# Optimization experiments

Hardware: AMD Instinct MI355X
Metric: run time of the kernel (lower is better)

## Reference

```python
import jax, jax.numpy as jnp
import numpy as np
from jax import lax

K_NEIGHBORS = 8  # num_neighbors
EPS_BN = 1e-5

def _bn(x, g, b, axes):
    # training-mode batch norm over `axes`, channel axis = 1
    m = jnp.mean(x, axis=axes, keepdims=True)
    v = jnp.var(x, axis=axes, keepdims=True)
    shp = [1] * x.ndim; shp[1] = x.shape[1]
    return (x - m) / jnp.sqrt(v + EPS_BN) * g.reshape(shp) + b.reshape(shp)

def _conv(x, w, b):
    y = lax.conv_general_dilated(x, w, (1, 1), 'SAME',
                                 dimension_numbers=('NCHW', 'OIHW', 'NCHW'))
    return y + b[None, :, None, None]

def setup_inputs() -> dict:
    key = jax.random.key(0)
    ks = jax.random.split(key, 20)
    B, C, H, W = 64, 200, 27, 27
    D, F, NC, HID = 64, 9, 16, 128
    inp = {
        'x': jax.random.normal(ks[0], (B, C, H, W), jnp.float32),
        'conv1_w': jax.random.normal(ks[1], (32, C, 3, 3), jnp.float32) * 0.02,
        'conv1_b': jnp.zeros((32,), jnp.float32),
        'bn1_g': jnp.ones((32,), jnp.float32), 'bn1_b': jnp.zeros((32,), jnp.float32),
        'conv2_w': jax.random.normal(ks[2], (64, 32, 3, 3), jnp.float32) * 0.05,
        'conv2_b': jnp.zeros((64,), jnp.float32),
        'bn2_g': jnp.ones((64,), jnp.float32), 'bn2_b': jnp.zeros((64,), jnp.float32),
        'conv3_w': jax.random.normal(ks[3], (D, 64, 3, 3), jnp.float32) * 0.05,
        'conv3_b': jnp.zeros((D,), jnp.float32),
        'bn3_g': jnp.ones((D,), jnp.float32), 'bn3_b': jnp.zeros((D,), jnp.float32),
        'w_self': jax.random.normal(ks[4], (D, D), jnp.float32) * (2.0 / (2 * D)) ** 0.5,
        'w_nb': jax.random.normal(ks[5], (D, D), jnp.float32) * (2.0 / (2 * D)) ** 0.5,
        'gkan_bias': jnp.zeros((D,), jnp.float32),
        'kan_a': jax.random.normal(ks[6], (D, 3), jnp.float32) * 0.1,
        'kan_b': jax.random.normal(ks[7], (D, 2), jnp.float32) * 0.1,
        'gkan_bn_g': jnp.ones((D,), jnp.float32), 'gkan_bn_b': jnp.zeros((D,), jnp.float32),
        'centers': jax.random.normal(ks[8], (D, F), jnp.float32),
        'gamma': jnp.ones((D, F), jnp.float32) * 0.5,
        'attn_w1': jax.random.normal(ks[9], (D // 4, D), jnp.float32) * 0.1,
        'attn_b1': jnp.zeros((D // 4,), jnp.float32),
        'attn_w2': jax.random.normal(ks[10], (D, D // 4), jnp.float32) * 0.1,
        'attn_b2': jnp.zeros((D,), jnp.float32),
        'fa_bn_g': jnp.ones((D,), jnp.float32), 'fa_bn_b': jnp.zeros((D,), jnp.float32),
        'fc1_w': jax.random.normal(ks[11], (HID, D), jnp.float32) * 0.1,
        'fc1_b': jnp.zeros((HID,), jnp.float32),
        'cls_bn_g': jnp.ones((HID,), jnp.float32), 'cls_bn_b': jnp.zeros((HID,), jnp.float32),
        'fc2_w': jax.random.normal(ks[12], (NC, HID), jnp.float32) * 0.1,
        'fc2_b': jnp.zeros((NC,), jnp.float32),
    }
    return inp

def _forward(x, conv1_w, conv1_b, bn1_g, bn1_b, conv2_w, conv2_b, bn2_g, bn2_b,
             conv3_w, conv3_b, bn3_g, bn3_b, w_self, w_nb, gkan_bias, kan_a, kan_b,
             gkan_bn_g, gkan_bn_b, centers, gamma, attn_w1, attn_b1, attn_w2, attn_b2,
             fa_bn_g, fa_bn_b, fc1_w, fc1_b, cls_bn_g, cls_bn_b, fc2_w, fc2_b):
    # --- CNN encoder ---
    h = jax.nn.relu(_bn(_conv(x, conv1_w, conv1_b), bn1_g, bn1_b, (0, 2, 3)))
    h = jax.nn.relu(_bn(_conv(h, conv2_w, conv2_b), bn2_g, bn2_b, (0, 2, 3)))
    h = jax.nn.relu(_bn(_conv(h, conv3_w, conv3_b), bn3_g, bn3_b, (0, 2, 3)))
    # --- tokenize: [B,D,H,W] -> [B,N,D] ---
    B, D, H, W = h.shape
    N = H * W
    t = h.reshape(B, D, N).transpose(0, 2, 1)
    # --- kNN graph (vectorized topk + scatter) ---
    xx = jnp.sum(t * t, axis=-1, keepdims=True)               # [B,N,1]
    xy = jnp.einsum('bnd,bmd->bnm', t, t)                     # [B,N,N]
    dist = jnp.maximum(xx - 2.0 * xy + xx.transpose(0, 2, 1), 0.0)
    k = min(K_NEIGHBORS + 1, N)
    _, idx = lax.top_k(-dist, k)                              # smallest-k, [B,N,k]
    adj = jnp.zeros((B, N, N), t.dtype).at[
        jnp.arange(B)[:, None, None], jnp.arange(N)[None, :, None], idx[:, :, 1:]
    ].set(1.0)
    deg = jnp.sum(adj, axis=-1) + 1e-6                        # [B,N]
    dinv = deg ** -0.5
    adj_norm = dinv[:, :, None] * adj * dinv[:, None, :] + jnp.eye(N, dtype=t.dtype)[None]
    # --- GKAN graph conv ---
    h_self = t @ w_self                                       # [B,N,D]
    h_nb = jnp.einsum('bnm,bmd->bnd', adj_norm, t @ w_nb)
    g = h_self + h_nb + gkan_bias
    g2 = g * g
    num = kan_a[:, 0] + kan_a[:, 1] * g + kan_a[:, 2] * g2
    den = 1.0 + jnp.abs(kan_b[:, 0] * g + kan_b[:, 1] * g2)
    g = num / (den + 1e-8)
    g = _bn(g.transpose(0, 2, 1), gkan_bn_g, gkan_bn_b, (0, 2)).transpose(0, 2, 1)
    # --- Fuzzy attention (RBF membership; logsumexp(log(v+1e-10)) == sum(v+1e-10)) ---
    d2 = (g[..., None] - centers[None, None]) ** 2            # [B,N,D,F]
    rbf = jnp.sum(jnp.exp(-jnp.abs(gamma)[None, None] * d2) + 1e-10, axis=-1)
    a1 = jax.nn.relu(rbf @ attn_w1.T + attn_b1)
    attn = jax.nn.sigmoid(a1 @ attn_w2.T + attn_b2)
    g = g * attn + g
    g = _bn(g.transpose(0, 2, 1), fa_bn_g, fa_bn_b, (0, 2)).transpose(0, 2, 1)
    # dropout: identity in eval
    # --- global pool + classifier ---
    p = 0.5 * jnp.mean(g, axis=1) + 0.5 * jnp.max(g, axis=1)  # [B,D]
    c = p @ fc1_w.T + fc1_b
    c = jax.nn.relu(_bn(c, cls_bn_g, cls_bn_b, (0,)))
    return c @ fc2_w.T + fc2_b

def reference(x, conv1_w, conv1_b, bn1_g, bn1_b, conv2_w, conv2_b, bn2_g, bn2_b,
              conv3_w, conv3_b, bn3_g, bn3_b, w_self, w_nb, gkan_bias, kan_a, kan_b,
              gkan_bn_g, gkan_bn_b, centers, gamma, attn_w1, attn_b1, attn_w2, attn_b2,
              fa_bn_g, fa_bn_b, fc1_w, fc1_b, cls_bn_g, cls_bn_b, fc2_w, fc2_b):
    return _forward(x, conv1_w, conv1_b, bn1_g, bn1_b, conv2_w, conv2_b, bn2_g, bn2_b,
                    conv3_w, conv3_b, bn3_g, bn3_b, w_self, w_nb, gkan_bias, kan_a, kan_b,
                    gkan_bn_g, gkan_bn_b, centers, gamma, attn_w1, attn_b1, attn_w2, attn_b2,
                    fa_bn_g, fa_bn_b, fc1_w, fc1_b, cls_bn_g, cls_bn_b, fc2_w, fc2_b)
```

## Files before the change

kernel.cpp:

```cpp
#include <hip/hip_runtime.h>
#include <math.h>

#define BATCH 64
#define NTOK  729
#define DIM   64
#define NROWS 46656

#define SROW 33
#define SCH  (29 * SROW)

template<int CIN_CHUNK, bool BN_IN>
__global__ __launch_bounds__(256) void conv3x3_v6(
    const float* __restrict__ in, const float* __restrict__ wgt,
    const float* __restrict__ scsh, float* __restrict__ outp,
    int Cin, int Cout, int cinPerSlab, int nslab)
{
  int bigGroups = Cout / 16;
  int blocksPerB = bigGroups * nslab;
  int b = blockIdx.x / blocksPerB;
  int rr = blockIdx.x % blocksPerB;
  int bg = rr / nslab;
  int slab = rr % nslab;
  int c_begin = slab * cinPerSlab;
  int c_end = c_begin + cinPerSlab; if (c_end > Cin) c_end = Cin;

  __shared__ float s_in[CIN_CHUNK * SCH + SROW];
  __shared__ float s_w[16 * CIN_CHUNK * 12];
  __shared__ float s_sc[CIN_CHUNK];
  __shared__ float s_sh[CIN_CHUNK];

  const int tid = threadIdx.x;
  const int grp = tid >> 7;
  const int idx = tid & 127;
  const bool active = idx < 126;
  const int rp = idx / 9;
  const int py = 2 * rp;
  const int px3 = (idx % 9) * 3;
  const bool row2ok = (py + 1) < 27;

  float acc[8][2][3];
  #pragma unroll
  for (int t = 0; t < 8; ++t)
    #pragma unroll
    for (int rI = 0; rI < 2; ++rI) { acc[t][rI][0]=0.f; acc[t][rI][1]=0.f; acc[t][rI][2]=0.f; }

  const size_t inB = (size_t)b * Cin;

  for (int i = tid; i < CIN_CHUNK * SCH + SROW; i += 256) s_in[i] = 0.f;

  for (int c0 = c_begin; c0 < c_end; c0 += CIN_CHUNK) {
    int ccn = c_end - c0; if (ccn > CIN_CHUNK) ccn = CIN_CHUNK;
    if (BN_IN && tid < ccn) {
      s_sc[tid] = scsh[c0 + tid];
      s_sh[tid] = scsh[Cin + c0 + tid];
    }
    __syncthreads();
    {
      const float* src = &in[(inB + c0) * 729];
      for (int i = tid; i < ccn * 729; i += 256) {
        int cc = i / 729; int rem = i - cc * 729;
        int y = rem / 27; int x = rem - y * 27;
        float v = src[i];
        if (BN_IN) v = fmaxf(fmaf(v, s_sc[cc], s_sh[cc]), 0.f);
        s_in[cc * SCH + (y + 1) * SROW + (x + 1)] = v;
      }
    }
    for (int i = tid; i < 16 * CIN_CHUNK * 9; i += 256) {
      int t = i / (CIN_CHUNK * 9); int r2 = i - t * CIN_CHUNK * 9;
      int cc = r2 / 9; int k = r2 - cc * 9;
      float wv = 0.f;
      if (cc < ccn) wv = wgt[((size_t)(bg * 16 + t) * Cin + (c0 + cc)) * 9 + k];
      s_w[(t * CIN_CHUNK + cc) * 12 + k] = wv;
    }
    __syncthreads();
    if (active) {
      #pragma unroll 1
      for (int cc = 0; cc < ccn; ++cc) {
        const float* bp = &s_in[cc * SCH + py * SROW + px3];
        float r0[5], r1[5], r2[5], r3[5];
        #pragma unroll
        for (int j = 0; j < 5; ++j) {
          r0[j] = bp[j];
          r1[j] = bp[SROW + j];
          r2[j] = bp[2*SROW + j];
          r3[j] = bp[3*SROW + j];
        }
        #pragma unroll
        for (int t = 0; t < 8; ++t) {
          const int wb = ((grp * 8 + t) * CIN_CHUNK + cc) * 12;
          const float4 wa = *(const float4*)&s_w[wb];
          const float4 wc = *(const float4*)&s_w[wb + 4];
          const float  w8 = s_w[wb + 8];
          #pragma unroll
          for (int p = 0; p < 3; ++p) {
            acc[t][0][p] += wa.x*r0[p]+wa.y*r0[p+1]+wa.z*r0[p+2]
                          + wa.w*r1[p]+wc.x*r1[p+1]+wc.y*r1[p+2]
                          + wc.z*r2[p]+wc.w*r2[p+1]+w8*r2[p+2];
            acc[t][1][p] += wa.x*r1[p]+wa.y*r1[p+1]+wa.z*r1[p+2]
                          + wa.w*r2[p]+wc.x*r2[p+1]+wc.y*r2[p+2]
                          + wc.z*r3[p]+wc.w*r3[p+1]+w8*r3[p+2];
          }
        }
      }
    }
  }
  if (active) {
    #pragma unroll
    for (int t = 0; t < 8; ++t) {
      size_t base = (((size_t)slab * BATCH + b) * Cout + (bg * 16 + grp * 8 + t)) * 729 + py * 27 + px3;
      outp[base+0]=acc[t][0][0]; outp[base+1]=acc[t][0][1]; outp[base+2]=acc[t][0][2];
      if (row2ok) {
        outp[base+27]=acc[t][1][0]; outp[base+28]=acc[t][1][1]; outp[base+29]=acc[t][1][2];
      }
    }
  }
}

__global__ __launch_bounds__(256) void conv_reduce_stats(
    const float* __restrict__ part, const float* __restrict__ bias,
    float* __restrict__ outp, double* __restrict__ stats, int C, int nslab)
{
  int b = blockIdx.x / C;
  int c = blockIdx.x % C;
  size_t slabStride = (size_t)BATCH * C * 729;
  size_t base = ((size_t)b * C + c) * 729;
  float bv = bias[c];
  float bsum = 0.f, bsq = 0.f;
  for (int e = threadIdx.x; e < 729; e += 256) {
    float v = bv;
    for (int s = 0; s < nslab; ++s) v += part[s*slabStride + base + e];
    outp[base + e] = v;
    bsum += v; bsq += v*v;
  }
  #pragma unroll
  for (int off = 32; off > 0; off >>= 1) {
    bsum += __shfl_down(bsum, off);
    bsq  += __shfl_down(bsq, off);
  }
  __shared__ float rs[4], rq[4];
  int wid = threadIdx.x >> 6;
  if ((threadIdx.x & 63) == 0) { rs[wid] = bsum; rq[wid] = bsq; }
  __syncthreads();
  if (threadIdx.x == 0) {
    float s1 = rs[0]+rs[1]+rs[2]+rs[3];
    float q1 = rq[0]+rq[1]+rq[2]+rq[3];
    atomicAdd(&stats[c], (double)s1);
    atomicAdd(&stats[C + c], (double)q1);
  }
}

__global__ void bn_finalize(const double* __restrict__ stats,
                            const float* __restrict__ gamma, const float* __restrict__ beta,
                            float* __restrict__ scsh, int C, float invCount)
{
  int c = threadIdx.x + blockIdx.x * blockDim.x; if (c >= C) return;
  double mu = stats[c] * (double)invCount;
  double var = stats[C + c] * (double)invCount - mu * mu;
  float rstd = (float)(1.0 / sqrt(var + 1e-5));
  float sc = gamma[c] * rstd;
  scsh[c] = sc;
  scsh[C + c] = beta[c] - (float)mu * sc;
}

__global__ __launch_bounds__(256) void bn_transpose_xx(
    const float* __restrict__ c3, const float* __restrict__ scsh,
    float* __restrict__ t, float* __restrict__ xx)
{
  int lb = (blockIdx.x & 7) * 96 + (blockIdx.x >> 3);
  int b = lb / 12, nt = lb % 12, n0 = nt * 64;
  __shared__ float s[64 * 65];
  for (int i = threadIdx.x; i < 4096; i += 256) {
    int d = i >> 6, j = i & 63; int n = n0 + j;
    float v = 0.f;
    if (n < 729) {
      v = c3[((size_t)b * 64 + d) * 729 + n];
      v = fmaxf(fmaf(v, scsh[d], scsh[64 + d]), 0.f);
    }
    s[d * 65 + j] = v;
  }
  __syncthreads();
  for (int i = threadIdx.x; i < 4096; i += 256) {
    int j = i >> 6, d = i & 63; int n = n0 + j;
    if (n < 729) t[((size_t)b * 729 + n) * 64 + d] = s[d * 65 + j];
  }
  if (threadIdx.x < 64) {
    int j = threadIdx.x; int n = n0 + j;
    if (n < 729) {
      float sm = 0.f;
      #pragma unroll
      for (int d = 0; d < 64; ++d) { float v = s[d * 65 + j]; sm += v * v; }
      xx[b * 729 + n] = sm;
    }
  }
}

__global__ __launch_bounds__(256) void gemm_selfnb(
    const float* __restrict__ t, const float* __restrict__ wself,
    const float* __restrict__ wnb, float* __restrict__ hs, float* __restrict__ hw)
{
  int lb = (blockIdx.x & 7) * 96 + (blockIdx.x >> 3);
  int b = lb / 12, nt = lb % 12, n0 = nt * 64;
  __shared__ __align__(16) float s_tT[64 * 68];
  __shared__ __align__(16) float s_a[64 * 68];
  __shared__ __align__(16) float s_b[64 * 68];
  const int tid = threadIdx.x;
  for (int i = tid; i < 1024; i += 256) {
    int n = i >> 4, dq = i & 15;
    float4 v = make_float4(0.f, 0.f, 0.f, 0.f);
    if (n0 + n < 729) v = *(const float4*)&t[((size_t)b * 729 + n0 + n) * 64 + 4 * dq];
    s_tT[(4*dq+0)*68 + n] = v.x;
    s_tT[(4*dq+1)*68 + n] = v.y;
    s_tT[(4*dq+2)*68 + n] = v.z;
    s_tT[(4*dq+3)*68 + n] = v.w;
  }
  for (int i = tid; i < 1024; i += 256) {
    int d = i >> 4, jq = i & 15;
    *(float4*)&s_a[d*68 + 4*jq] = *(const float4*)&wself[d*64 + 4*jq];
    *(float4*)&s_b[d*68 + 4*jq] = *(const float4*)&wnb[d*64 + 4*jq];
  }
  __syncthreads();
  int ty = tid >> 4, tx = tid & 15;
  float acc0[4][4], acc1[4][4];
  #pragma unroll
  for (int i = 0; i < 4; ++i)
    #pragma unroll
    for (int j = 0; j < 4; ++j) { acc0[i][j] = 0.f; acc1[i][j] = 0.f; }
  #pragma unroll 8
  for (int d = 0; d < 64; ++d) {
    float4 av = *(const float4*)&s_tT[d*68 + 4*ty];
    float4 b1 = *(const float4*)&s_a[d*68 + 4*tx];
    float4 b2 = *(const float4*)&s_b[d*68 + 4*tx];
    float a[4] = {av.x, av.y, av.z, av.w};
    float u[4] = {b1.x, b1.y, b1.z, b1.w};
    float w[4] = {b2.x, b2.y, b2.z, b2.w};
    #pragma unroll
    for (int i = 0; i < 4; ++i)
      #pragma unroll
      for (int j = 0; j < 4; ++j) { acc0[i][j] += a[i]*u[j]; acc1[i][j] += a[i]*w[j]; }
  }
  #pragma unroll
  for (int i = 0; i < 4; ++i) {
    int n = n0 + 4*ty + i;
    if (n < 729) {
      size_t o = ((size_t)b * 729 + n) * 64 + 4*tx;
      *(float4*)&hs[o] = make_float4(acc0[i][0], acc0[i][1], acc0[i][2], acc0[i][3]);
      *(float4*)&hw[o] = make_float4(acc1[i][0], acc1[i][1], acc1[i][2], acc1[i][3]);
    }
  }
}

__global__ __launch_bounds__(256) void dist_topk(
    const float* __restrict__ t, const float* __restrict__ xx, int* __restrict__ nbr)
{
  int lb = (blockIdx.x & 7) * 96 + (blockIdx.x >> 3);
  int b = lb / 12, nt = lb % 12, n0 = nt * 64;
  __shared__ __align__(16) float s_nT[64 * 68];
  __shared__ __align__(16) float s_m0[64 * 68];
  __shared__ __align__(16) float s_m1[64 * 68];

  const int tid = threadIdx.x;
  const int rg = tid >> 3;
  const int cg = tid & 7;
  const int r0 = 2 * rg, r1 = r0 + 1;
  const int self0 = n0 + r0, self1 = n0 + r1;
  const size_t tb = (size_t)b * 729;
  const float* xxb = &xx[b * 729];

  float kv0[8], kv1[8]; int ki0[8], ki1[8];
  #pragma unroll
  for (int i = 0; i < 8; ++i) {
    kv0[i] = 3.0e38f; ki0[i] = 0x7fffffff;
    kv1[i] = 3.0e38f; ki1[i] = 0x7fffffff;
  }

  for (int i = tid; i < 1024; i += 256) {
    int n = i >> 4, dq = i & 15;
    float4 v = make_float4(0.f, 0.f, 0.f, 0.f);
    if (n0 + n < 729) v = *(const float4*)&t[(tb + n0 + n) * 64 + 4 * dq];
    s_nT[(4*dq+0)*68 + n] = v.x;
    s_nT[(4*dq+1)*68 + n] = v.y;
    s_nT[(4*dq+2)*68 + n] = v.z;
    s_nT[(4*dq+3)*68 + n] = v.w;
  }
  for (int i = tid; i < 1024; i += 256) {
    int m = i >> 4, dq = i & 15;
    float4 v = *(const float4*)&t[(tb + m) * 64 + 4 * dq];
    s_m0[(4*dq+0)*68 + m] = v.x;
    s_m0[(4*dq+1)*68 + m] = v.y;
    s_m0[(4*dq+2)*68 + m] = v.z;
    s_m0[(4*dq+3)*68 + m] = v.w;
  }
  __syncthreads();

  for (int mt = 0; mt < 12; ++mt) {
    const int m0 = mt * 64;
    const float* cur = (mt & 1) ? s_m1 : s_m0;
    float*       nxt = (mt & 1) ? s_m0 : s_m1;

    float4 st[4];
    if (mt < 11) {
      #pragma unroll
      for (int j = 0; j < 4; ++j) {
        int i = tid + 256 * j; int m = i >> 4, dq = i & 15;
        int mm = m0 + 64 + m;
        st[j] = (mm < 729) ? *(const float4*)&t[(tb + mm) * 64 + 4 * dq]
                           : make_float4(0.f, 0.f, 0.f, 0.f);
      }
    }
    float xm[8];
    #pragma unroll
    for (int k = 0; k < 8; ++k) {
      xm[k] = xxb[m0 + 8*cg + k];
    }

    float acc0[8], acc1[8];
    #pragma unroll
    for (int j = 0; j < 8; ++j) { acc0[j] = 0.f; acc1[j] = 0.f; }
    #pragma unroll 4
    for (int d = 0; d < 64; ++d) {
      float2 a  = *(const float2*)&s_nT[d*68 + r0];
      float4 bA = *(const float4*)&cur[d*68 + 8*cg];
      float4 bB = *(const float4*)&cur[d*68 + 8*cg + 4];
      float bb[8] = {bA.x, bA.y, bA.z, bA.w, bB.x, bB.y, bB.z, bB.w};
      #pragma unroll
      for (int j = 0; j < 8; ++j) {
        acc0[j] += a.x * bb[j];
        acc1[j] += a.y * bb[j];
      }
    }

    #pragma unroll
    for (int k = 0; k < 8; ++k) {
      int m = m0 + 8*cg + k;
      bool inb = (m < 729);
      {
        float sv = fmaf(-2.f, acc0[k], xm[k]);
        bool lt = inb && (m != self0) &&
                  ((sv < kv0[7]) || (sv == kv0[7] && m < ki0[7]));
        if (lt) {
          float cv = sv; int ci = m;
          #pragma unroll
          for (int ii = 0; ii < 8; ++ii) {
            bool less = (cv < kv0[ii]) || (cv == kv0[ii] && ci < ki0[ii]);
            float tv = less ? kv0[ii] : cv; int ti = less ? ki0[ii] : ci;
            kv0[ii] = less ? cv : kv0[ii]; ki0[ii] = less ? ci : ki0[ii];
            cv = tv; ci = ti;
          }
        }
      }
      {
        float sv = fmaf(-2.f, acc1[k], xm[k]);
        bool lt = inb && (m != self1) &&
                  ((sv < kv1[7]) || (sv == kv1[7] && m < ki1[7]));
        if (lt) {
          float cv = sv; int ci = m;
          #pragma unroll
          for (int ii = 0; ii < 8; ++ii) {
            bool less = (cv < kv1[ii]) || (cv == kv1[ii] && ci < ki1[ii]);
            float tv = less ? kv1[ii] : cv; int ti = less ? ki1[ii] : ci;
            kv1[ii] = less ? cv : kv1[ii]; ki1[ii] = less ? ci : ki1[ii];
            cv = tv; ci = ti;
          }
        }
      }
    }

    if (mt < 11) {
      #pragma unroll
      for (int j = 0; j < 4; ++j) {
        int i = tid + 256 * j; int m = i >> 4, dq = i & 15;
        nxt[(4*dq+0)*68 + m] = st[j].x;
        nxt[(4*dq+1)*68 + m] = st[j].y;
        nxt[(4*dq+2)*68 + m] = st[j].z;
        nxt[(4*dq+3)*68 + m] = st[j].w;
      }
    }
    __syncthreads();
  }

  float* mv = s_m0;
  int*   mi = (int*)s_m1;
  #pragma unroll
  for (int k = 0; k < 8; ++k) {
    mv[r0*68 + cg*8 + k] = kv0[k]; mi[r0*68 + cg*8 + k] = ki0[k];
    mv[r1*68 + cg*8 + k] = kv1[k]; mi[r1*68 + cg*8 + k] = ki1[k];
  }
  __syncthreads();
  if (tid < 64) {
    int n = n0 + tid;
    if (n < 729) {
      int rb = tid * 68;
      int p[8] = {0,0,0,0,0,0,0,0};
      int* op = &nbr[((size_t)b * 729 + n) * 8];
      for (int o = 0; o < 8; ++o) {
        float bvv = 3.5e38f; int bii = 0x7fffffff; int bq = 0;
        #pragma unroll
        for (int q = 0; q < 8; ++q) {
          float v = mv[rb + q*8 + p[q]]; int ii = mi[rb + q*8 + p[q]];
          if (v < bvv || (v == bvv && ii < bii)) { bvv = v; bii = ii; bq = q; }
        }
        #pragma unroll
        for (int q = 0; q < 8; ++q) p[q] += (bq == q);
        op[o] = bii;
      }
    }
  }
}

__global__ __launch_bounds__(256) void gkan_kernel(
    const float* __restrict__ hs, const float* __restrict__ hw,
    const int* __restrict__ nbr, const float* __restrict__ bias,
    const float* __restrict__ kan_a, const float* __restrict__ kan_b,
    float* __restrict__ gpre)
{
  int row = blockIdx.x * 4 + (threadIdx.x >> 6);
  int d = threadIdx.x & 63;
  float degf = 8.0f + 1e-6f;
  float coef = 1.0f / degf;
  size_t bbase = (size_t)(row / 729) * 729;
  float v = hs[(size_t)row * 64 + d] + hw[(size_t)row * 64 + d] + bias[d];
  float nsum = 0.f;
  #pragma unroll
  for (int j = 0; j < 8; ++j) {
    int m = nbr[(size_t)row * 8 + j];
    nsum += hw[(bbase + m) * 64 + d];
  }
  v += coef * nsum;
  float a0 = kan_a[d*3], a1 = kan_a[d*3+1], a2 = kan_a[d*3+2];
  float b0 = kan_b[d*2], b1 = kan_b[d*2+1];
  float v2 = v * v;
  float num = a0 + a1*v + a2*v2;
  float den = 1.f + fabsf(b0*v + b1*v2);
  gpre[(size_t)row * 64 + d] = num / (den + 1e-8f);
}

__global__ __launch_bounds__(256) void stats_tok(
    const float* __restrict__ g, double* __restrict__ stats)
{
  int d = threadIdx.x & 63, qq = threadIdx.x >> 6;
  int r0 = blockIdx.x * 183;
  int rend = r0 + 183; if (rend > NROWS) rend = NROWS;
  float sm = 0.f, sq = 0.f;
  for (int r = r0 + qq; r < rend; r += 4) {
    float v = g[(size_t)r * 64 + d];
    sm += v; sq += v * v;
  }
  __shared__ float ls[256], lq[256];
  ls[threadIdx.x] = sm; lq[threadIdx.x] = sq;
  __syncthreads();
  if (threadIdx.x < 64) {
    sm = ls[d] + ls[64+d] + ls[128+d] + ls[192+d];
    sq = lq[d] + lq[64+d] + lq[128+d] + lq[192+d];
    atomicAdd(&stats[d], (double)sm);
    atomicAdd(&stats[64 + d], (double)sq);
  }
}

__global__ __launch_bounds__(256) void fuzzy_attn(
    const float* __restrict__ gpre, const float* __restrict__ scshG,
    const float* __restrict__ centers, const float* __restrict__ gam,
    const float* __restrict__ w1, const float* __restrict__ b1,
    const float* __restrict__ w2, const float* __restrict__ b2,
    float* __restrict__ g2)
{
  int wv = threadIdx.x >> 6, d = threadIdx.x & 63;
  int row = blockIdx.x * 4 + wv;
  __shared__ float s_rbf[4][64];
  __shared__ float s_a1[4][16];
  float v = gpre[(size_t)row * 64 + d];
  float gn = fmaf(v, scshG[d], scshG[64 + d]);
  float acc = 0.f;
  #pragma unroll
  for (int f = 0; f < 9; ++f) {
    float dc = gn - centers[d*9 + f];
    acc += expf(-fabsf(gam[d*9 + f]) * dc * dc);
  }
  s_rbf[wv][d] = acc + 9e-10f;
  __syncthreads();
  if (d < 16) {
    float a = b1[d];
    #pragma unroll 8
    for (int k = 0; k < 64; ++k) a += w1[d*64 + k] * s_rbf[wv][k];
    s_a1[wv][d] = fmaxf(a, 0.f);
  }
  __syncthreads();
  float a2 = b2[d];
  #pragma unroll
  for (int i = 0; i < 16; ++i) a2 += w2[d*16 + i] * s_a1[wv][i];
  float sig = 1.f / (1.f + expf(-a2));
  g2[(size_t)row * 64 + d] = gn * (1.f + sig);
}

__global__ __launch_bounds__(256) void pool_kernel(
    const float* __restrict__ g2, const float* __restrict__ scshF, float* __restrict__ p)
{
  int b = blockIdx.x;
  int d = threadIdx.x & 63, qq = threadIdx.x >> 6;
  float sc = scshF[d], sh = scshF[64 + d];
  float sm = 0.f, mx = -3.0e38f;
  for (int n = qq; n < 729; n += 4) {
    float v = fmaf(g2[((size_t)b * 729 + n) * 64 + d], sc, sh);
    sm += v; mx = fmaxf(mx, v);
  }
  __shared__ float ls[256], lm[256];
  ls[threadIdx.x] = sm; lm[threadIdx.x] = mx;
  __syncthreads();
  if (threadIdx.x < 64) {
    sm = ls[d] + ls[64+d] + ls[128+d] + ls[192+d];
    mx = fmaxf(fmaxf(lm[d], lm[64+d]), fmaxf(lm[128+d], lm[192+d]));
    p[b * 64 + d] = 0.5f * (sm / 729.f) + 0.5f * mx;
  }
}

__global__ __launch_bounds__(256) void classifier(
    const float* __restrict__ p, const float* __restrict__ f1w, const float* __restrict__ f1b,
    const float* __restrict__ bng, const float* __restrict__ bnb,
    const float* __restrict__ f2w, const float* __restrict__ f2b, float* __restrict__ outp)
{
  __shared__ float s_p[64 * 64];
  __shared__ float s_c[64 * 128];
  __shared__ float s_sc[128], s_sh[128];
  for (int i = threadIdx.x; i < 4096; i += 256) s_p[i] = p[i];
  __syncthreads();
  for (int o = threadIdx.x; o < 8192; o += 256) {
    int b = o >> 7, h = o & 127;
    float acc = f1b[h];
    #pragma unroll 8
    for (int d = 0; d < 64; ++d) acc += s_p[b*64 + d] * f1w[h*64 + d];
    s_c[o] = acc;
  }
  __syncthreads();
  if (threadIdx.x < 128) {
    int h = threadIdx.x;
    float sm = 0.f, sq = 0.f;
    for (int b = 0; b < 64; ++b) { float v = s_c[b*128 + h]; sm += v; sq += v*v; }
    float mu = sm / 64.f;
    float var = sq / 64.f - mu * mu;
    float rstd = rsqrtf(var + 1e-5f);
    float sc = bng[h] * rstd;
    s_sc[h] = sc; s_sh[h] = bnb[h] - mu * sc;
  }
  __syncthreads();
  for (int o = threadIdx.x; o < 1024; o += 256) {
    int b = o >> 4, j = o & 15;
    float acc = f2b[j];
    #pragma unroll 8
    for (int h = 0; h < 128; ++h) {
      float v = fmaxf(fmaf(s_c[b*128 + h], s_sc[h], s_sh[h]), 0.f);
      acc += f2w[j*128 + h] * v;
    }
    outp[o] = acc;
  }
}

extern "C" void kernel_launch(void* const* d_in, const int* in_sizes, int n_in,
                              void* d_out, int out_size, void* d_ws, size_t ws_size,
                              hipStream_t stream)
{
  const float* x      = (const float*)d_in[0];
  const float* c1w    = (const float*)d_in[1];
  const float* c1b    = (const float*)d_in[2];
  const float* bn1g   = (const float*)d_in[3];
  const float* bn1b   = (const float*)d_in[4];
  const float* c2wt   = (const float*)d_in[5];
  const float* c2b    = (const float*)d_in[6];
  const float* bn2g   = (const float*)d_in[7];
  const float* bn2b   = (const float*)d_in[8];
  const float* c3wt   = (const float*)d_in[9];
  const float* c3b    = (const float*)d_in[10];
  const float* bn3g   = (const float*)d_in[11];
  const float* bn3b   = (const float*)d_in[12];
  const float* wself  = (const float*)d_in[13];
  const float* wnb    = (const float*)d_in[14];
  const float* gbias  = (const float*)d_in[15];
  const float* kana   = (const float*)d_in[16];
  const float* kanb   = (const float*)d_in[17];
  const float* gbng   = (const float*)d_in[18];
  const float* gbnb   = (const float*)d_in[19];
  const float* cent   = (const float*)d_in[20];
  const float* gamr   = (const float*)d_in[21];
  const float* aw1    = (const float*)d_in[22];
  const float* ab1    = (const float*)d_in[23];
  const float* aw2    = (const float*)d_in[24];
  const float* ab2    = (const float*)d_in[25];
  const float* fbng   = (const float*)d_in[26];
  const float* fbnb   = (const float*)d_in[27];
  const float* f1w    = (const float*)d_in[28];
  const float* f1b    = (const float*)d_in[29];
  const float* cbng   = (const float*)d_in[30];
  const float* cbnb   = (const float*)d_in[31];
  const float* f2w    = (const float*)d_in[32];
  const float* f2b    = (const float*)d_in[33];

  const size_t BIG_NEED = 79338496;
  const bool big = (ws_size >= BIG_NEED);

  char* ws = (char*)d_ws;
  size_t Psz = big ? 47775744u : 23887872u;
  float*  P     = (float*) (ws + 0);
  float*  c1    = (float*) (ws + Psz);
  float*  c2    = (float*) (ws + Psz + 5971968);
  float*  c3    = (float*) (ws + Psz + 17915904);
  int*    nbr   = (int*)   (ws + Psz + 29859840);
  float*  xx    = (float*) (ws + Psz + 31352832);
  double* stats = (double*)(ws + Psz + 31539456);
  float*  scsh  = (float*) (ws + Psz + 31544064);
  float*  pbuf  = (float*) (ws + Psz + 31546368);
  float* hw   = P;
  float* t    = (float*)(ws + 11943936);
  float* hs   = c2;
  float* gpre = c3;
  float* g2   = t;

  const int ns1 = big ? 8 : 4, cps1 = big ? 25 : 50;
  const int ns2 = big ? 4 : 2, cps2 = big ? 8  : 16;
  const int ns3 = big ? 4 : 2, cps3 = big ? 16 : 32;
  const int g1 = 2 * ns1 * 64;
  const int g2r = 4 * ns2 * 64;
  const int g3 = 4 * ns3 * 64;

  hipMemsetAsync(stats, 0, 576 * sizeof(double), stream);

  const float inv = 1.0f / 46656.0f;

  conv3x3_v6<8,false><<<dim3(g1), dim3(256), 0, stream>>>(
      x,  c1w, nullptr, P, 200, 32, cps1, ns1);
  conv_reduce_stats<<<dim3(2048), dim3(256), 0, stream>>>(P, c1b, c1, stats, 32, ns1);
  bn_finalize<<<dim3(1), dim3(32), 0, stream>>>(stats, bn1g, bn1b, scsh, 32, inv);
  conv3x3_v6<8,true><<<dim3(g2r), dim3(256), 0, stream>>>(
      c1, c2wt, scsh, P, 32, 64, cps2, ns2);
  conv_reduce_stats<<<dim3(4096), dim3(256), 0, stream>>>(P, c2b, c2, stats + 64, 64, ns2);
  bn_finalize<<<dim3(1), dim3(64), 0, stream>>>(stats + 64, bn2g, bn2b, scsh + 64, 64, inv);
  conv3x3_v6<8,true><<<dim3(g3), dim3(256), 0, stream>>>(
      c2, c3wt, scsh + 64, P, 64, 64, cps3, ns3);
  conv_reduce_stats<<<dim3(4096), dim3(256), 0, stream>>>(P, c3b, c3, stats + 192, 64, ns3);
  bn_finalize<<<dim3(1), dim3(64), 0, stream>>>(stats + 192, bn3g, bn3b, scsh + 192, 64, inv);
  bn_transpose_xx<<<dim3(768), dim3(256), 0, stream>>>(c3, scsh + 192, t, xx);
  gemm_selfnb<<<dim3(768), dim3(256), 0, stream>>>(t, wself, wnb, hs, hw);
  dist_topk<<<dim3(768), dim3(256), 0, stream>>>(t, xx, nbr);
  gkan_kernel<<<dim3(11664), dim3(256), 0, stream>>>(hs, hw, nbr, gbias, kana, kanb, gpre);
  stats_tok<<<dim3(256), dim3(256), 0, stream>>>(gpre, stats + 320);
  bn_finalize<<<dim3(1), dim3(64), 0, stream>>>(stats + 320, gbng, gbnb, scsh + 320, 64, inv);
  fuzzy_attn<<<dim3(11664), dim3(256), 0, stream>>>(gpre, scsh + 320, cent, gamr, aw1, ab1, aw2, ab2, g2);
  stats_tok<<<dim3(256), dim3(256), 0, stream>>>(g2, stats + 448);
  bn_finalize<<<dim3(1), dim3(64), 0, stream>>>(stats + 448, fbng, fbnb, scsh + 448, 64, inv);
  pool_kernel<<<dim3(64), dim3(256), 0, stream>>>(g2, scsh + 448, pbuf);
  classifier<<<dim3(1), dim3(256), 0, stream>>>(pbuf, f1w, f1b, cbng, cbnb, f2w, f2b, (float*)d_out);
}
```

Baseline: 809.7 us.

## Fuse BN finalize into stats kernels, swizzle topk LDS, parallelize attn hidden layer

Replaces the five separate single-block bn_finalize launches with a last-block-done ticket inside the stats reduction kernels, which removes kernel launch gaps. It also XOR-swizzles the shared-memory layout in dist_topk to cut LDS bank conflicts, and spreads the 16-wide attention hidden layer across all 64 lanes with shuffle reductions. In exchange it adds ticket counters and a larger memset, and relies on threadfence plus atomic reads being correct.

Result: slower. 987.7 us (+22.0%).

```diff
diff --git a/kernel.cpp b/kernel.cpp
--- a/kernel.cpp
+++ b/kernel.cpp
@@ -116,9 +116,11 @@
   }
 }
 
-__global__ __launch_bounds__(256) void conv_reduce_stats(
+__global__ __launch_bounds__(256) void conv_reduce_stats_fin(
     const float* __restrict__ part, const float* __restrict__ bias,
-    float* __restrict__ outp, double* __restrict__ stats, int C, int nslab)
+    float* __restrict__ outp, double* __restrict__ stats, int C, int nslab,
+    const float* __restrict__ gamma, const float* __restrict__ beta,
+    float* __restrict__ scshOut, int* __restrict__ ticket, float invCount)
 {
   int b = blockIdx.x / C;
   int c = blockIdx.x % C;
@@ -138,6 +140,7 @@
     bsq  += __shfl_down(bsq, off);
   }
   __shared__ float rs[4], rq[4];
+  __shared__ int isLast;
   int wid = threadIdx.x >> 6;
   if ((threadIdx.x & 63) == 0) { rs[wid] = bsum; rq[wid] = bsq; }
   __syncthreads();
@@ -146,20 +149,21 @@
     float q1 = rq[0]+rq[1]+rq[2]+rq[3];
     atomicAdd(&stats[c], (double)s1);
     atomicAdd(&stats[C + c], (double)q1);
-  }
-}
-
-__global__ void bn_finalize(const double* __restrict__ stats,
-                            const float* __restrict__ gamma, const float* __restrict__ beta,
-                            float* __restrict__ scsh, int C, float invCount)
-{
-  int c = threadIdx.x + blockIdx.x * blockDim.x; if (c >= C) return;
-  double mu = stats[c] * (double)invCount;
-  double var = stats[C + c] * (double)invCount - mu * mu;
-  float rstd = (float)(1.0 / sqrt(var + 1e-5));
-  float sc = gamma[c] * rstd;
-  scsh[c] = sc;
-  scsh[C + c] = beta[c] - (float)mu * sc;
+    __threadfence();
+    isLast = (atomicAdd(ticket, 1) == (int)gridDim.x - 1) ? 1 : 0;
+  }
+  __syncthreads();
+  if (isLast && threadIdx.x < C) {
+    int cc = threadIdx.x;
+    double s = atomicAdd(&stats[cc], 0.0);
+    double q = atomicAdd(&stats[C + cc], 0.0);
+    double mu = s * (double)invCount;
+    double var = q * (double)invCount - mu * mu;
+    float rstd = (float)(1.0 / sqrt(var + 1e-5));
+    float sc = gamma[cc] * rstd;
+    scshOut[cc] = sc;
+    scshOut[C + cc] = beta[cc] - (float)mu * sc;
+  }
 }
 
 __global__ __launch_bounds__(256) void bn_transpose_xx(
@@ -277,18 +281,22 @@
     int n = i >> 4, dq = i & 15;
     float4 v = make_float4(0.f, 0.f, 0.f, 0.f);
     if (n0 + n < 729) v = *(const float4*)&t[(tb + n0 + n) * 64 + 4 * dq];
-    s_nT[(4*dq+0)*68 + n] = v.x;
-    s_nT[(4*dq+1)*68 + n] = v.y;
-    s_nT[(4*dq+2)*68 + n] = v.z;
-    s_nT[(4*dq+3)*68 + n] = v.w;
+    int xr = (4 * dq) & 56;
+    int ns = n ^ xr;
+    s_nT[(4*dq+0)*68 + ns] = v.x;
+    s_nT[(4*dq+1)*68 + ns] = v.y;
+    s_nT[(4*dq+2)*68 + ns] = v.z;
+    s_nT[(4*dq+3)*68 + ns] = v.w;
   }
   for (int i = tid; i < 1024; i += 256) {
     int m = i >> 4, dq = i & 15;
     float4 v = *(const float4*)&t[(tb + m) * 64 + 4 * dq];
-    s_m0[(4*dq+0)*68 + m] = v.x;
-    s_m0[(4*dq+1)*68 + m] = v.y;
-    s_m0[(4*dq+2)*68 + m] = v.z;
-    s_m0[(4*dq+3)*68 + m] = v.w;
+    int xr = (4 * dq) & 56;
+    int ms = m ^ xr;
+    s_m0[(4*dq+0)*68 + ms] = v.x;
+    s_m0[(4*dq+1)*68 + ms] = v.y;
+    s_m0[(4*dq+2)*68 + ms] = v.z;
+    s_m0[(4*dq+3)*68 + ms] = v.w;
   }
   __syncthreads();
 
@@ -318,9 +326,11 @@
     for (int j = 0; j < 8; ++j) { acc0[j] = 0.f; acc1[j] = 0.f; }
     #pragma unroll 4
     for (int d = 0; d < 64; ++d) {
-      float2 a  = *(const float2*)&s_nT[d*68 + r0];
-      float4 bA = *(const float4*)&cur[d*68 + 8*cg];
-      float4 bB = *(const float4*)&cur[d*68 + 8*cg + 4];
+      int dx = d & 56;
+      float2 a  = *(const float2*)&s_nT[d*68 + (r0 ^ dx)];
+      int bc = (8*cg) ^ dx;
+      float4 bA = *(const float4*)&cur[d*68 + bc];
+      float4 bB = *(const float4*)&cur[d*68 + bc + 4];
       float bb[8] = {bA.x, bA.y, bA.z, bA.w, bB.x, bB.y, bB.z, bB.w};
       #pragma unroll
       for (int j = 0; j < 8; ++j) {
@@ -369,10 +379,12 @@
       #pragma unroll
       for (int j = 0; j < 4; ++j) {
         int i = tid + 256 * j; int m = i >> 4, dq = i & 15;
-        nxt[(4*dq+0)*68 + m] = st[j].x;
-        nxt[(4*dq+1)*68 + m] = st[j].y;
-        nxt[(4*dq+2)*68 + m] = st[j].z;
-        nxt[(4*dq+3)*68 + m] = st[j].w;
+        int xr = (4 * dq) & 56;
+        int ms = m ^ xr;
+        nxt[(4*dq+0)*68 + ms] = st[j].x;
+        nxt[(4*dq+1)*68 + ms] = st[j].y;
+        nxt[(4*dq+2)*68 + ms] = st[j].z;
+        nxt[(4*dq+3)*68 + ms] = st[j].w;
       }
     }
     __syncthreads();
@@ -434,8 +446,10 @@
   gpre[(size_t)row * 64 + d] = num / (den + 1e-8f);
 }
 
-__global__ __launch_bounds__(256) void stats_tok(
-    const float* __restrict__ g, double* __restrict__ stats)
+__global__ __launch_bounds__(256) void stats_tok_fin(
+    const float* __restrict__ g, double* __restrict__ stats,
+    const float* __restrict__ gamma, const float* __restrict__ beta,
+    float* __restrict__ scshOut, int* __restrict__ ticket, float invCount)
 {
   int d = threadIdx.x & 63, qq = threadIdx.x >> 6;
   int r0 = blockIdx.x * 183;
@@ -446,6 +460,7 @@
     sm += v; sq += v * v;
   }
   __shared__ float ls[256], lq[256];
+  __shared__ int isLast;
   ls[threadIdx.x] = sm; lq[threadIdx.x] = sq;
   __syncthreads();
   if (threadIdx.x < 64) {
@@ -453,6 +468,22 @@
     sq = lq[d] + lq[64+d] + lq[128+d] + lq[192+d];
     atomicAdd(&stats[d], (double)sm);
     atomicAdd(&stats[64 + d], (double)sq);
+  }
+  __threadfence();
+  __syncthreads();
+  if (threadIdx.x == 0)
+    isLast = (atomicAdd(ticket, 1) == (int)gridDim.x - 1) ? 1 : 0;
+  __syncthreads();
+  if (isLast && threadIdx.x < 64) {
+    int cc = threadIdx.x;
+    double s = atomicAdd(&stats[cc], 0.0);
+    double q = atomicAdd(&stats[64 + cc], 0.0);
+    double mu = s * (double)invCount;
+    double var = q * (double)invCount - mu * mu;
+    float rstd = (float)(1.0 / sqrt(var + 1e-5));
+    float sc = gamma[cc] * rstd;
+    scshOut[cc] = sc;
+    scshOut[64 + cc] = beta[cc] - (float)mu * sc;
   }
 }
 
@@ -477,11 +508,16 @@
   }
   s_rbf[wv][d] = acc + 9e-10f;
   __syncthreads();
-  if (d < 16) {
-    float a = b1[d];
-    #pragma unroll 8
-    for (int k = 0; k < 64; ++k) a += w1[d*64 + k] * s_rbf[wv][k];
-    s_a1[wv][d] = fmaxf(a, 0.f);
+  {
+    int h = d >> 2, s = d & 3;
+    const float* wrow = &w1[h * 64 + s * 16];
+    const float* rb = &s_rbf[wv][s * 16];
+    float a = 0.f;
+    #pragma unroll
+    for (int k = 0; k < 16; ++k) a += wrow[k] * rb[k];
+    a += __shfl_xor(a, 1);
+    a += __shfl_xor(a, 2);
+    if (s == 0) s_a1[wv][h] = fmaxf(a + b1[h], 0.f);
   }
   __syncthreads();
   float a2 = b2[d];
@@ -592,7 +628,7 @@
   const float* f2w    = (const float*)d_in[32];
   const float* f2b    = (const float*)d_in[33];
 
-  const size_t BIG_NEED = 79338496;
+  const size_t BIG_NEED = 79338528;
   const bool big = (ws_size >= BIG_NEED);
 
   char* ws = (char*)d_ws;
@@ -606,6 +642,7 @@
   double* stats = (double*)(ws + Psz + 31539456);
   float*  scsh  = (float*) (ws + Psz + 31544064);
   float*  pbuf  = (float*) (ws + Psz + 31546368);
+  int*    tick  = (int*)   (ws + Psz + 31562752);
   float* hw   = P;
   float* t    = (float*)(ws + 11943936);
   float* hs   = c2;
@@ -619,31 +656,31 @@
   const int g2r = 4 * ns2 * 64;
   const int g3 = 4 * ns3 * 64;
 
-  hipMemsetAsync(stats, 0, 576 * sizeof(double), stream);
+  hipMemsetAsync(stats, 0, 4608 + 2304 + 16384 + 32, stream);
 
   const float inv = 1.0f / 46656.0f;
 
   conv3x3_v6<8,false><<<dim3(g1), dim3(256), 0, stream>>>(
       x,  c1w, nullptr, P, 200, 32, cps1, ns1);
-  conv_reduce_stats<<<dim3(2048), dim3(256), 0, stream>>>(P, c1b, c1, stats, 32, ns1);
-  bn_finalize<<<dim3(1), dim3(32), 0, stream>>>(stats, bn1g, bn1b, scsh, 32, inv);
+  conv_reduce_stats_fin<<<dim3(2048), dim3(256), 0, stream>>>(
+      P, c1b, c1, stats, 32, ns1, bn1g, bn1b, scsh, tick + 0, inv);
   conv3x3_v6<8,true><<<dim3(g2r), dim3(256), 0, stream>>>(
       c1, c2wt, scsh, P, 32, 64, cps2, ns2);
-  conv_reduce_stats<<<dim3(4096), dim3(256), 0, stream>>>(P, c2b, c2, stats + 64, 64, ns2);
-  bn_finalize<<<dim3(1), dim3(64), 0, stream>>>(stats + 64, bn2g, bn2b, scsh + 64, 64, inv);
+  conv_reduce_stats_fin<<<dim3(4096), dim3(256), 0, stream>>>(
+      P, c2b, c2, stats + 64, 64, ns2, bn2g, bn2b, scsh + 64, tick + 1, inv);
   conv3x3_v6<8,true><<<dim3(g3), dim3(256), 0, stream>>>(
       c2, c3wt, scsh + 64, P, 64, 64, cps3, ns3);
-  conv_reduce_stats<<<dim3(4096), dim3(256), 0, stream>>>(P, c3b, c3, stats + 192, 64, ns3);
-  bn_finalize<<<dim3(1), dim3(64), 0, stream>>>(stats + 192, bn3g, bn3b, scsh + 192, 64, inv);
+  conv_reduce_stats_fin<<<dim3(4096), dim3(256), 0, stream>>>(
+      P, c3b, c3, stats + 192, 64, ns3, bn3g, bn3b, scsh + 192, tick + 2, inv);
   bn_transpose_xx<<<dim3(768), dim3(256), 0, stream>>>(c3, scsh + 192, t, xx);
   gemm_selfnb<<<dim3(768), dim3(256), 0, stream>>>(t, wself, wnb, hs, hw);
   dist_topk<<<dim3(768), dim3(256), 0, stream>>>(t, xx, nbr);
   gkan_kernel<<<dim3(11664), dim3(256), 0, stream>>>(hs, hw, nbr, gbias, kana, kanb, gpre);
-  stats_tok<<<dim3(256), dim3(256), 0, stream>>>(gpre, stats + 320);
-  bn_finalize<<<dim3(1), dim3(64), 0, stream>>>(stats + 320, gbng, gbnb, scsh + 320, 64, inv);
+  stats_tok_fin<<<dim3(256), dim3(256), 0, stream>>>(
+      gpre, stats + 320, gbng, gbnb, scsh + 320, tick + 3, inv);
   fuzzy_attn<<<dim3(11664), dim3(256), 0, stream>>>(gpre, scsh + 320, cent, gamr, aw1, ab1, aw2, ab2, g2);
-  stats_tok<<<dim3(256), dim3(256), 0, stream>>>(g2, stats + 448);
-  bn_finalize<<<dim3(1), dim3(64), 0, stream>>>(stats + 448, fbng, fbnb, scsh + 448, 64, inv);
+  stats_tok_fin<<<dim3(256), dim3(256), 0, stream>>>(
+      g2, stats + 448, fbng, fbnb, scsh + 448, tick + 4, inv);
   pool_kernel<<<dim3(64), dim3(256), 0, stream>>>(g2, scsh + 448, pbuf);
   classifier<<<dim3(1), dim3(256), 0, stream>>>(pbuf, f1w, f1b, cbng, cbnb, f2w, f2b, (float*)d_out);
 }
```
